# Optimization experiments

Measured on AMD Instinct MI355X. Metric: run time of the kernel, lower is better.

Reference implementation:

```python
import jax, jax.numpy as jnp
import numpy as np
import math

EPS = 1e-3  # numerical_stabilizer in relu_kernel_transformation


def setup_inputs() -> dict:
    key = jax.random.key(0)
    ks = jax.random.split(key, 6)
    B, L, DIM = 8, 4096, 768
    H, D, M = 12, 64, 256
    x = jax.random.normal(ks[0], (B, L, DIM), dtype=jnp.float32)
    qkv_w = jax.random.normal(ks[1], (3 * DIM, DIM), dtype=jnp.float32) * (DIM ** -0.5)
    qkv_b = jnp.zeros((3 * DIM,), dtype=jnp.float32)
    proj_w = jax.random.normal(ks[2], (DIM, DIM), dtype=jnp.float32) * (DIM ** -0.5)
    proj_b = jnp.zeros((DIM,), dtype=jnp.float32)
    # Gaussian orthogonal random matrix [M, D] (blocks of orthogonal rows, chi-scaled)
    blocks = []
    for i in range(M // D):
        g = jax.random.normal(ks[3 + 0] if False else jax.random.fold_in(ks[3], i), (D, D), dtype=jnp.float32)
        q, _ = jnp.linalg.qr(g)
        blocks.append(q.T)
    pm = jnp.concatenate(blocks, axis=0)  # [M, D]
    mult = jnp.linalg.norm(jax.random.normal(ks[4], (M, D), dtype=jnp.float32), axis=1)
    proj_mat = mult[:, None] * pm
    return {"x": x, "qkv_w": qkv_w, "qkv_b": qkv_b,
            "proj_w": proj_w, "proj_b": proj_b, "proj_mat": proj_mat}


def _relu_features(t, proj_mat):
    # t: [B, L, H, D], proj_mat: [M, D] -> [B, L, H, M]
    ratio = 1.0 / math.sqrt(float(proj_mat.shape[0]))
    z = ratio * jnp.einsum('blhd,md->blhm', t, proj_mat)
    return jax.nn.relu(z) + EPS


def reference(x, qkv_w, qkv_b, proj_w, proj_b, proj_mat):
    B, L, DIM = x.shape
    H = 12
    D = DIM // H
    qkv = x @ qkv_w.T + qkv_b                      # [B, L, 3*DIM]
    qkv = qkv.reshape(B, L, 3, H, D)
    q, k, v = qkv[:, :, 0], qkv[:, :, 1], qkv[:, :, 2]   # [B, L, H, D]
    q_p = _relu_features(q, proj_mat)              # [B, L, H, M]
    k_p = _relu_features(k, proj_mat)              # [B, L, H, M]
    # Non-causal FAVOR+ linear attention
    kv = jnp.einsum('blhm,blhd->bhmd', k_p, v)     # [B, H, M, D]
    k_sum = k_p.sum(axis=1)                        # [B, H, M]
    num = jnp.einsum('blhm,bhmd->blhd', q_p, kv)   # [B, L, H, D]
    den = jnp.einsum('blhm,bhm->blh', q_p, k_sum)  # [B, L, H]
    out = num / den[..., None]
    out = out.reshape(B, L, DIM)
    return out @ proj_w.T + proj_b
```

## Files before the change

kernel.cpp:

```cpp
#include <hip/hip_runtime.h>
#include <hip/hip_bf16.h>
#include <cstdint>

typedef __hip_bfloat16 bf16;
typedef short bf16x8 __attribute__((ext_vector_type(8)));
typedef float f32x4 __attribute__((ext_vector_type(4)));

#define RATIO 0.0625f
#define EPS_F 0.001f

__device__ __forceinline__ void unpack8(uint4 u, float* f) {
  f[0] = __uint_as_float(u.x << 16); f[1] = __uint_as_float(u.x & 0xffff0000u);
  f[2] = __uint_as_float(u.y << 16); f[3] = __uint_as_float(u.y & 0xffff0000u);
  f[4] = __uint_as_float(u.z << 16); f[5] = __uint_as_float(u.z & 0xffff0000u);
  f[6] = __uint_as_float(u.w << 16); f[7] = __uint_as_float(u.w & 0xffff0000u);
}

__device__ __forceinline__ unsigned short f2bf(float f) {
  unsigned int u = __float_as_uint(f);
  unsigned int r = (u + 0x7fffu + ((u >> 16) & 1u)) >> 16;
  return (unsigned short)r;
}

__device__ __forceinline__ void gload_lds16(const void* g, void* l) {
  __builtin_amdgcn_global_load_lds(
      (const __attribute__((address_space(1))) void*)(uintptr_t)g,
      (__attribute__((address_space(3))) void*)(uintptr_t)l, 16, 0, 0);
}

__global__ void zero_kernel(float* __restrict__ p, int n) {
  int i = blockIdx.x * 256 + threadIdx.x;
  if (i < n) p[i] = 0.f;
}

__global__ void conv_kernel(const float* __restrict__ src,
                            unsigned short* __restrict__ dst, long n) {
  long i = ((long)blockIdx.x * 256 + threadIdx.x) * 4;
  if (i < n) {
    float4 v = *(const float4*)(src + i);
    ushort4 o;
    o.x = f2bf(v.x); o.y = f2bf(v.y); o.z = f2bf(v.z); o.w = f2bf(v.w);
    *(ushort4*)(dst + i) = o;
  }
}

__device__ __forceinline__ void ds_read_B8(const short* Bb, int rB0, int l16,
                                           int quad, bf16x8 bfr[4][2]) {
  const int sw = l16 & 7;
#pragma unroll
  for (int ni = 0; ni < 4; ++ni)
#pragma unroll
    for (int ks = 0; ks < 2; ++ks)
      bfr[ni][ks] = *(const bf16x8*)
          &Bb[(rB0 + ni * 16 + l16) * 64 + (((ks * 4 + quad) ^ sw) * 8)];
}

template <int Q>
__device__ __forceinline__ void ds_read_A4(const short* Ab, int l16, int quad,
                                           bf16x8 af[2][2]) {
  const int sw = l16 & 7;
#pragma unroll
  for (int i = 0; i < 2; ++i)
#pragma unroll
    for (int ks = 0; ks < 2; ++ks)
      af[i][ks] = *(const bf16x8*)
          &Ab[((Q * 2 + i) * 16 + l16) * 64 + (((ks * 4 + quad) ^ sw) * 8)];
}

template <int Q>
__device__ __forceinline__ void mfma16(f32x4 acc[8][4], bf16x8 af[2][2],
                                       bf16x8 bfr[4][2]) {
#pragma unroll
  for (int i = 0; i < 2; ++i)
#pragma unroll
    for (int ni = 0; ni < 4; ++ni)
#pragma unroll
      for (int ks = 0; ks < 2; ++ks)
        acc[Q * 2 + i][ni] = __builtin_amdgcn_mfma_f32_16x16x32_bf16(
            af[i][ks], bfr[ni][ks], acc[Q * 2 + i][ni], 0, 0, 0);
}

template <bool OUT_F32>
__global__ __launch_bounds__(512, 2) void gemm_bt_kernel(
    const bf16* __restrict__ A, const bf16* __restrict__ Bt,
    const float* __restrict__ bias, void* __restrict__ Cout,
    int Ndim, int Kdim)
{
  __shared__ short lds[65536];
  const int tid = threadIdx.x;
  const int lane = tid & 63;
  const int w = tid >> 6;
  const int wr = w >> 2;
  const int wc = w & 3;
  const int quad = lane >> 4, l16 = lane & 15;

  int gx = gridDim.x;
  int nwg = gx * gridDim.y;
  int flat = blockIdx.y * gx + blockIdx.x;
  int qq = nwg >> 3, rr = nwg & 7;
  int xcd = flat & 7, sub = flat >> 3;
  int wg = (xcd < rr ? xcd * (qq + 1) : rr * (qq + 1) + (xcd - rr) * qq) + sub;
  long m0 = (long)(wg / gx) * 256;
  long n0 = (long)(wg % gx) * 256;

  const int r8 = lane >> 3;
  const int csw = ((lane & 7) ^ (r8 & 7)) * 8;
  const bf16* gAs = A + (m0 + (w >> 2) * 128 + (w & 3) * 8 + r8) * (long)Kdim + csw;
  const bf16* gBs = Bt + (n0 + w * 8 + r8) * (long)Kdim + csw;
  short* dA = &lds[(w >> 2) * 8192 + (w & 3) * 512];
  short* dB = &lds[32768 + w * 512];
  const long kb64 = 64L * Kdim;
  const long ka32 = 32L * Kdim;

  f32x4 acc[8][4];
#pragma unroll
  for (int i = 0; i < 8; i++)
#pragma unroll
    for (int j = 0; j < 4; j++)
      acc[i][j] = (f32x4){0.f, 0.f, 0.f, 0.f};

  const int NIT = Kdim >> 6;

#pragma unroll
  for (int j = 0; j < 4; ++j) gload_lds16(gBs + j * kb64, dB + j * 4096);
#pragma unroll
  for (int qa = 0; qa < 4; ++qa) gload_lds16(gAs + qa * ka32, dA + qa * 2048);
  asm volatile("s_waitcnt vmcnt(3)" ::: "memory");
  __builtin_amdgcn_s_barrier();

  bf16x8 bfr[4][2], af[2][2];

  for (int it = 0; it < NIT; ++it) {
    const int d = it & 1, nd = d ^ 1;
    const bool pf = (it < NIT - 1);
    const long kq1 = (long)(it + 1) * 64;
    const short* Ab = &lds[d * 16384 + wr * 8192];
    const short* Bb = &lds[32768 + d * 16384 + (wc >> 1) * 8192];
    const int rB0 = (wc & 1) * 64;
    short* dAn = dA + nd * 16384;
    short* dBn = dB + nd * 16384;

    ds_read_B8(Bb, rB0, l16, quad, bfr);
    ds_read_A4<0>(Ab, l16, quad, af);
    if (pf) {
      gload_lds16(gBs + kq1, dBn);
      gload_lds16(gBs + kb64 + kq1, dBn + 4096);
      asm volatile("s_waitcnt vmcnt(4)" ::: "memory");
    } else {
      asm volatile("s_waitcnt vmcnt(2)" ::: "memory");
    }
    asm volatile("s_waitcnt lgkmcnt(8)" ::: "memory");
    __builtin_amdgcn_s_barrier();
    asm volatile("s_waitcnt lgkmcnt(0)" ::: "memory");
    __builtin_amdgcn_sched_barrier(0);
    __builtin_amdgcn_s_setprio(1);
    mfma16<0>(acc, af, bfr);
    __builtin_amdgcn_s_setprio(0);
    __builtin_amdgcn_s_barrier();

    ds_read_A4<1>(Ab, l16, quad, af);
    if (pf) {
      gload_lds16(gBs + 2 * kb64 + kq1, dBn + 8192);
      gload_lds16(gBs + 3 * kb64 + kq1, dBn + 12288);
      asm volatile("s_waitcnt vmcnt(5)" ::: "memory");
    } else {
      asm volatile("s_waitcnt vmcnt(1)" ::: "memory");
    }
    __builtin_amdgcn_s_barrier();
    asm volatile("s_waitcnt lgkmcnt(0)" ::: "memory");
    __builtin_amdgcn_sched_barrier(0);
    __builtin_amdgcn_s_setprio(1);
    mfma16<1>(acc, af, bfr);
    __builtin_amdgcn_s_setprio(0);
    __builtin_amdgcn_s_barrier();

    ds_read_A4<2>(Ab, l16, quad, af);
    if (pf) {
      gload_lds16(gAs + kq1, dAn);
      gload_lds16(gAs + ka32 + kq1, dAn + 2048);
      asm volatile("s_waitcnt vmcnt(6)" ::: "memory");
    } else {
      asm volatile("s_waitcnt vmcnt(0)" ::: "memory");
    }
    __builtin_amdgcn_s_barrier();
    asm volatile("s_waitcnt lgkmcnt(0)" ::: "memory");
    __builtin_amdgcn_sched_barrier(0);
    __builtin_amdgcn_s_setprio(1);
    mfma16<2>(acc, af, bfr);
    __builtin_amdgcn_s_setprio(0);
    __builtin_amdgcn_s_barrier();

    ds_read_A4<3>(Ab, l16, quad, af);
    if (pf) {
      gload_lds16(gAs + 2 * ka32 + kq1, dAn + 4096);
      gload_lds16(gAs + 3 * ka32 + kq1, dAn + 6144);
      asm volatile("s_waitcnt vmcnt(3)" ::: "memory");
    }
    __builtin_amdgcn_s_barrier();
    asm volatile("s_waitcnt lgkmcnt(0)" ::: "memory");
    __builtin_amdgcn_sched_barrier(0);
    __builtin_amdgcn_s_setprio(1);
    mfma16<3>(acc, af, bfr);
    __builtin_amdgcn_s_setprio(0);
    __builtin_amdgcn_s_barrier();
  }

#pragma unroll
  for (int ni = 0; ni < 4; ++ni) {
    long col = n0 + wc * 64 + ni * 16 + l16;
    float bv = bias[col];
#pragma unroll
    for (int mi = 0; mi < 8; ++mi) {
      long row = m0 + wr * 128 + mi * 16 + quad * 4;
#pragma unroll
      for (int r = 0; r < 4; ++r) {
        float val = acc[mi][ni][r] + bv;
        if (OUT_F32)
          ((float*)Cout)[(row + r) * Ndim + col] = val;
        else
          ((bf16*)Cout)[(row + r) * Ndim + col] = __float2bfloat16(val);
      }
    }
  }
}

__global__ __launch_bounds__(256) void kv_mfma_kernel(
    const bf16* __restrict__ qkv, const bf16* __restrict__ pmb,
    float* __restrict__ kvbuf, float* __restrict__ ksumb)
{
  int bh = blockIdx.x;
  int b = bh / 12, h = bh % 12;
  int l0 = blockIdx.y * 1024;
  int tid = threadIdx.x, lane = tid & 63, w = tid >> 6;
  int quad = lane >> 4, l16 = lane & 15;

  __shared__ short k_lds[64 * 72];
  __shared__ short v_lds[64 * 72];
  __shared__ short kp3[256 * 72];

  f32x4 kvacc[4][4];
#pragma unroll
  for (int mt = 0; mt < 4; mt++)
#pragma unroll
    for (int dt = 0; dt < 4; dt++)
      kvacc[mt][dt] = (f32x4){0.f, 0.f, 0.f, 0.f};
  float ksum_r = 0.f;

  int srow = tid >> 2, sseg = (tid & 3) * 8;
  int swz = ((srow >> 3) & 3) << 4;

  for (int tile = 0; tile < 16; tile++) {
    long gr = ((long)(b * 4096 + l0 + tile * 64 + srow)) * 2304 + h * 64;
    uint4 kk0 = *(const uint4*)(qkv + gr + 768 + sseg);
    uint4 kk1 = *(const uint4*)(qkv + gr + 768 + sseg + 32);
    uint4 vv0 = *(const uint4*)(qkv + gr + 1536 + sseg);
    uint4 vv1 = *(const uint4*)(qkv + gr + 1536 + sseg + 32);
    __syncthreads();
    *(uint4*)&k_lds[srow * 72 + sseg] = kk0;
    *(uint4*)&k_lds[srow * 72 + sseg + 32] = kk1;
    *(uint4*)&v_lds[srow * 72 + (sseg ^ swz)] = vv0;
    *(uint4*)&v_lds[srow * 72 + ((sseg + 32) ^ swz)] = vv1;
    __syncthreads();

    bf16x8 af[4][2], bpm[4][2];
#pragma unroll
    for (int lt = 0; lt < 4; lt++)
#pragma unroll
      for (int ks = 0; ks < 2; ks++)
        af[lt][ks] = *(const bf16x8*)&k_lds[(lt * 16 + l16) * 72 + ks * 32 + quad * 8];
#pragma unroll
    for (int mt = 0; mt < 4; mt++)
#pragma unroll
      for (int ks = 0; ks < 2; ks++)
        bpm[mt][ks] = *(const bf16x8*)(pmb + (w * 64 + mt * 16 + l16) * 64 + ks * 32 + quad * 8);

#pragma unroll
    for (int lt = 0; lt < 4; lt++)
#pragma unroll
      for (int mt = 0; mt < 4; mt++) {
        f32x4 s = (f32x4){0.f, 0.f, 0.f, 0.f};
        s = __builtin_amdgcn_mfma_f32_16x16x32_bf16(af[lt][0], bpm[mt][0], s, 0, 0, 0);
        s = __builtin_amdgcn_mfma_f32_16x16x32_bf16(af[lt][1], bpm[mt][1], s, 0, 0, 0);
        ushort4 pk;
        pk.x = f2bf(fmaxf(s[0] * RATIO, 0.f) + EPS_F);
        pk.y = f2bf(fmaxf(s[1] * RATIO, 0.f) + EPS_F);
        pk.z = f2bf(fmaxf(s[2] * RATIO, 0.f) + EPS_F);
        pk.w = f2bf(fmaxf(s[3] * RATIO, 0.f) + EPS_F);
        *(ushort4*)&kp3[(w * 64 + mt * 16 + l16) * 72 + lt * 16 + quad * 4] = pk;
      }
    __syncthreads();

#pragma unroll
    for (int j8 = 0; j8 < 8; j8++) {
      uint4 u = *(const uint4*)&kp3[tid * 72 + j8 * 8];
      float f[8]; unpack8(u, f);
      ksum_r += ((f[0] + f[1]) + (f[2] + f[3])) + ((f[4] + f[5]) + (f[6] + f[7]));
    }

#pragma unroll
    for (int ls = 0; ls < 2; ls++) {
      bf16x8 a2[4];
#pragma unroll
      for (int mt = 0; mt < 4; mt++)
        a2[mt] = *(const bf16x8*)&kp3[(w * 64 + mt * 16 + l16) * 72 + ls * 32 + quad * 8];
#pragma unroll
      for (int dt = 0; dt < 4; dt++) {
        bf16x8 b2;
        int dcol = (dt * 16 + l16) ^ (quad << 4);
#pragma unroll
        for (int jj = 0; jj < 8; jj++)
          b2[jj] = v_lds[(ls * 32 + quad * 8 + jj) * 72 + dcol];
#pragma unroll
        for (int mt = 0; mt < 4; mt++)
          kvacc[mt][dt] = __builtin_amdgcn_mfma_f32_16x16x32_bf16(a2[mt], b2, kvacc[mt][dt], 0, 0, 0);
      }
    }
  }

#pragma unroll
  for (int mt = 0; mt < 4; mt++)
#pragma unroll
    for (int dt = 0; dt < 4; dt++)
#pragma unroll
      for (int r = 0; r < 4; r++)
        atomicAdd(kvbuf + ((long)bh * 64 + dt * 16 + l16) * 256 + w * 64 + mt * 16 + quad * 4 + r,
                  kvacc[mt][dt][r]);
  atomicAdd(ksumb + bh * 256 + tid, ksum_r);
}

__global__ __launch_bounds__(256) void attn_mfma_kernel(
    const bf16* __restrict__ qkv, const bf16* __restrict__ pmb,
    const bf16* __restrict__ kvtb, const float* __restrict__ ksumb,
    bf16* __restrict__ attn)
{
  int bh = blockIdx.x;
  int b = bh / 12, h = bh % 12;
  int l0 = blockIdx.y * 64;
  int tid = threadIdx.x, lane = tid & 63, w = tid >> 6;
  int quad = lane >> 4, l16 = lane & 15;

  __shared__ short q_lds[64 * 72];
  __shared__ short qp2[64 * 264];
  __shared__ short kvt_lds[64 * 264];
  __shared__ float ksum_lds[256];
  __shared__ float den_part[4][64];

  {
    int srow = tid >> 2, sseg = (tid & 3) * 8;
    long gr = ((long)(b * 4096 + l0 + srow)) * 2304 + h * 64;
    *(uint4*)&q_lds[srow * 72 + sseg]      = *(const uint4*)(qkv + gr + sseg);
    *(uint4*)&q_lds[srow * 72 + sseg + 32] = *(const uint4*)(qkv + gr + sseg + 32);
  }
  {
    int row = tid >> 2, cb = (tid & 3) * 64;
    const bf16* src = kvtb + (long)bh * 16384 + row * 256 + cb;
    short* dst = &kvt_lds[row * 264 + cb];
#pragma unroll
    for (int j = 0; j < 8; j++)
      *(uint4*)(dst + j * 8) = *(const uint4*)(src + j * 8);
  }
  ksum_lds[tid] = ksumb[bh * 256 + tid];
  __syncthreads();

  {
    bf16x8 apm[4][2], bq[4][2];
#pragma unroll
    for (int mt = 0; mt < 4; mt++)
#pragma unroll
      for (int ks = 0; ks < 2; ks++)
        apm[mt][ks] = *(const bf16x8*)(pmb + (w * 64 + mt * 16 + l16) * 64 + ks * 32 + quad * 8);
#pragma unroll
    for (int lt = 0; lt < 4; lt++)
#pragma unroll
      for (int ks = 0; ks < 2; ks++)
        bq[lt][ks] = *(const bf16x8*)&q_lds[(lt * 16 + l16) * 72 + ks * 32 + quad * 8];

#pragma unroll
    for (int mt = 0; mt < 4; mt++)
#pragma unroll
      for (int lt = 0; lt < 4; lt++) {
        f32x4 s = (f32x4){0.f, 0.f, 0.f, 0.f};
        s = __builtin_amdgcn_mfma_f32_16x16x32_bf16(apm[mt][0], bq[lt][0], s, 0, 0, 0);
        s = __builtin_amdgcn_mfma_f32_16x16x32_bf16(apm[mt][1], bq[lt][1], s, 0, 0, 0);
        ushort4 pk;
        pk.x = f2bf(fmaxf(s[0] * RATIO, 0.f) + EPS_F);
        pk.y = f2bf(fmaxf(s[1] * RATIO, 0.f) + EPS_F);
        pk.z = f2bf(fmaxf(s[2] * RATIO, 0.f) + EPS_F);
        pk.w = f2bf(fmaxf(s[3] * RATIO, 0.f) + EPS_F);
        *(ushort4*)&qp2[(lt * 16 + l16) * 264 + w * 64 + mt * 16 + quad * 4] = pk;
      }
  }
  __syncthreads();

  {
    int l = tid & 63, Q = tid >> 6;
    float dp = 0.f;
#pragma unroll
    for (int j8 = 0; j8 < 8; j8++) {
      uint4 u = *(const uint4*)&qp2[l * 264 + Q * 64 + j8 * 8];
      float f[8]; unpack8(u, f);
#pragma unroll
      for (int i = 0; i < 8; i++) dp += f[i] * ksum_lds[Q * 64 + j8 * 8 + i];
    }
    den_part[Q][l] = dp;
  }

  f32x4 o[4];
#pragma unroll
  for (int dt = 0; dt < 4; dt++) o[dt] = (f32x4){0.f, 0.f, 0.f, 0.f};
#pragma unroll
  for (int ms = 0; ms < 8; ms++) {
    bf16x8 aq = *(const bf16x8*)&qp2[(w * 16 + l16) * 264 + ms * 32 + quad * 8];
#pragma unroll
    for (int dt = 0; dt < 4; dt++) {
      bf16x8 bk = *(const bf16x8*)&kvt_lds[(dt * 16 + l16) * 264 + ms * 32 + quad * 8];
      o[dt] = __builtin_amdgcn_mfma_f32_16x16x32_bf16(aq, bk, o[dt], 0, 0, 0);
    }
  }
  __syncthreads();

  float rden[4];
#pragma unroll
  for (int r = 0; r < 4; r++) {
    int l = w * 16 + quad * 4 + r;
    rden[r] = 1.f / (den_part[0][l] + den_part[1][l] + den_part[2][l] + den_part[3][l]);
  }
#pragma unroll
  for (int dt = 0; dt < 4; dt++)
#pragma unroll
    for (int r = 0; r < 4; r++) {
      int l = w * 16 + quad * 4 + r;
      attn[((long)(b * 4096 + l0 + l)) * 768 + h * 64 + dt * 16 + l16] =
          __float2bfloat16(o[dt][r] * rden[r]);
    }
}

extern "C" void kernel_launch(void* const* d_in, const int* in_sizes, int n_in,
                              void* d_out, int out_size, void* d_ws, size_t ws_size,
                              hipStream_t stream)
{
  const float* x      = (const float*)d_in[0];
  const float* qkv_w  = (const float*)d_in[1];
  const float* qkv_b  = (const float*)d_in[2];
  const float* proj_w = (const float*)d_in[3];
  const float* proj_b = (const float*)d_in[4];
  const float* pmat   = (const float*)d_in[5];
  float* out = (float*)d_out;

  char* ws = (char*)d_ws;
  bf16*  qkv   = (bf16*)ws;
  bf16*  xbuf  = (bf16*)(ws + 150994944);
  bf16*  attn  = xbuf;
  float* kvbuf = (float*)(ws + 201326592);
  float* ksumb = (float*)(ws + 207618048);
  bf16*  wqkv  = (bf16*)(ws + 207716352);
  bf16*  kvtb  = (bf16*)(ws + 207716352);
  bf16*  pmb   = (bf16*)(ws + 210862080);
  bf16*  wproj = (bf16*)(ws + 211255296);

  int nz = 96 * 64 * 256 + 96 * 256;
  zero_kernel<<<dim3((nz + 255) / 256), 256, 0, stream>>>(kvbuf, nz);

  conv_kernel<<<dim3(25165824 / 1024), 256, 0, stream>>>(x, (unsigned short*)xbuf, 25165824L);
  conv_kernel<<<dim3(1769472 / 1024), 256, 0, stream>>>(qkv_w, (unsigned short*)wqkv, 1769472L);
  conv_kernel<<<dim3(589824 / 1024), 256, 0, stream>>>(proj_w, (unsigned short*)wproj, 589824L);

  gemm_bt_kernel<false><<<dim3(2304 / 256, 32768 / 256), 512, 0, stream>>>(
      xbuf, wqkv, qkv_b, qkv, 2304, 768);

  conv_kernel<<<dim3(16384 / 1024), 256, 0, stream>>>(pmat, (unsigned short*)pmb, 16384L);

  kv_mfma_kernel<<<dim3(96, 4), 256, 0, stream>>>(qkv, pmb, kvbuf, ksumb);

  conv_kernel<<<dim3(1572864 / 1024), 256, 0, stream>>>(kvbuf, (unsigned short*)kvtb, 1572864L);

  attn_mfma_kernel<<<dim3(96, 64), 256, 0, stream>>>(qkv, pmb, kvtb, ksumb, attn);

  gemm_bt_kernel<true><<<dim3(768 / 256, 32768 / 256), 512, 0, stream>>>(
      attn, wproj, proj_b, out, 768, 768);
}
```

Measured before the change: 609.5 us.

## Split KV reduction over feature blocks instead of sequence chunks, drop atomics

```diff
diff --git a/kernel.cpp b/kernel.cpp
--- a/kernel.cpp
+++ b/kernel.cpp
@@ -26,11 +26,6 @@
   __builtin_amdgcn_global_load_lds(
       (const __attribute__((address_space(1))) void*)(uintptr_t)g,
       (__attribute__((address_space(3))) void*)(uintptr_t)l, 16, 0, 0);
-}
-
-__global__ void zero_kernel(float* __restrict__ p, int n) {
-  int i = blockIdx.x * 256 + threadIdx.x;
-  if (i < n) p[i] = 0.f;
 }
 
 __global__ void conv_kernel(const float* __restrict__ src,
@@ -230,27 +225,33 @@
 {
   int bh = blockIdx.x;
   int b = bh / 12, h = bh % 12;
-  int l0 = blockIdx.y * 1024;
+  int mb = blockIdx.y * 64;
   int tid = threadIdx.x, lane = tid & 63, w = tid >> 6;
   int quad = lane >> 4, l16 = lane & 15;
 
   __shared__ short k_lds[64 * 72];
   __shared__ short v_lds[64 * 72];
-  __shared__ short kp3[256 * 72];
-
-  f32x4 kvacc[4][4];
+  __shared__ short kp3[64 * 72];
+  __shared__ float red[4][64];
+
+  bf16x8 bpm[4][2];
 #pragma unroll
   for (int mt = 0; mt < 4; mt++)
 #pragma unroll
-    for (int dt = 0; dt < 4; dt++)
-      kvacc[mt][dt] = (f32x4){0.f, 0.f, 0.f, 0.f};
+    for (int ks = 0; ks < 2; ks++)
+      bpm[mt][ks] = *(const bf16x8*)(pmb + (mb + mt * 16 + l16) * 64 + ks * 32 + quad * 8);
+
+  f32x4 kvacc[4];
+#pragma unroll
+  for (int mt = 0; mt < 4; mt++) kvacc[mt] = (f32x4){0.f, 0.f, 0.f, 0.f};
   float ksum_r = 0.f;
 
   int srow = tid >> 2, sseg = (tid & 3) * 8;
   int swz = ((srow >> 3) & 3) << 4;
-
-  for (int tile = 0; tile < 16; tile++) {
-    long gr = ((long)(b * 4096 + l0 + tile * 64 + srow)) * 2304 + h * 64;
+  int mm = tid & 63, lq = tid >> 6;
+
+  for (int tile = 0; tile < 64; tile++) {
+    long gr = ((long)(b * 4096 + tile * 64 + srow)) * 2304 + h * 64;
     uint4 kk0 = *(const uint4*)(qkv + gr + 768 + sseg);
     uint4 kk1 = *(const uint4*)(qkv + gr + 768 + sseg + 32);
     uint4 vv0 = *(const uint4*)(qkv + gr + 1536 + sseg);
@@ -262,37 +263,29 @@
     *(uint4*)&v_lds[srow * 72 + ((sseg + 32) ^ swz)] = vv1;
     __syncthreads();
 
-    bf16x8 af[4][2], bpm[4][2];
-#pragma unroll
-    for (int lt = 0; lt < 4; lt++)
+    {
+      bf16x8 af[2];
 #pragma unroll
       for (int ks = 0; ks < 2; ks++)
-        af[lt][ks] = *(const bf16x8*)&k_lds[(lt * 16 + l16) * 72 + ks * 32 + quad * 8];
-#pragma unroll
-    for (int mt = 0; mt < 4; mt++)
-#pragma unroll
-      for (int ks = 0; ks < 2; ks++)
-        bpm[mt][ks] = *(const bf16x8*)(pmb + (w * 64 + mt * 16 + l16) * 64 + ks * 32 + quad * 8);
-
-#pragma unroll
-    for (int lt = 0; lt < 4; lt++)
+        af[ks] = *(const bf16x8*)&k_lds[(w * 16 + l16) * 72 + ks * 32 + quad * 8];
 #pragma unroll
       for (int mt = 0; mt < 4; mt++) {
         f32x4 s = (f32x4){0.f, 0.f, 0.f, 0.f};
-        s = __builtin_amdgcn_mfma_f32_16x16x32_bf16(af[lt][0], bpm[mt][0], s, 0, 0, 0);
-        s = __builtin_amdgcn_mfma_f32_16x16x32_bf16(af[lt][1], bpm[mt][1], s, 0, 0, 0);
+        s = __builtin_amdgcn_mfma_f32_16x16x32_bf16(af[0], bpm[mt][0], s, 0, 0, 0);
+        s = __builtin_amdgcn_mfma_f32_16x16x32_bf16(af[1], bpm[mt][1], s, 0, 0, 0);
         ushort4 pk;
         pk.x = f2bf(fmaxf(s[0] * RATIO, 0.f) + EPS_F);
         pk.y = f2bf(fmaxf(s[1] * RATIO, 0.f) + EPS_F);
         pk.z = f2bf(fmaxf(s[2] * RATIO, 0.f) + EPS_F);
         pk.w = f2bf(fmaxf(s[3] * RATIO, 0.f) + EPS_F);
-        *(ushort4*)&kp3[(w * 64 + mt * 16 + l16) * 72 + lt * 16 + quad * 4] = pk;
+        *(ushort4*)&kp3[(mt * 16 + l16) * 72 + w * 16 + quad * 4] = pk;
       }
+    }
     __syncthreads();
 
 #pragma unroll
-    for (int j8 = 0; j8 < 8; j8++) {
-      uint4 u = *(const uint4*)&kp3[tid * 72 + j8 * 8];
+    for (int j = 0; j < 2; j++) {
+      uint4 u = *(const uint4*)&kp3[mm * 72 + lq * 16 + j * 8];
       float f[8]; unpack8(u, f);
       ksum_r += ((f[0] + f[1]) + (f[2] + f[3])) + ((f[4] + f[5]) + (f[6] + f[7]));
     }
@@ -302,30 +295,30 @@
       bf16x8 a2[4];
 #pragma unroll
       for (int mt = 0; mt < 4; mt++)
-        a2[mt] = *(const bf16x8*)&kp3[(w * 64 + mt * 16 + l16) * 72 + ls * 32 + quad * 8];
-#pragma unroll
-      for (int dt = 0; dt < 4; dt++) {
-        bf16x8 b2;
-        int dcol = (dt * 16 + l16) ^ (quad << 4);
-#pragma unroll
-        for (int jj = 0; jj < 8; jj++)
-          b2[jj] = v_lds[(ls * 32 + quad * 8 + jj) * 72 + dcol];
-#pragma unroll
-        for (int mt = 0; mt < 4; mt++)
-          kvacc[mt][dt] = __builtin_amdgcn_mfma_f32_16x16x32_bf16(a2[mt], b2, kvacc[mt][dt], 0, 0, 0);
-      }
+        a2[mt] = *(const bf16x8*)&kp3[(mt * 16 + l16) * 72 + ls * 32 + quad * 8];
+      bf16x8 b2;
+      int dcol = (w * 16 + l16) ^ (quad << 4);
+#pragma unroll
+      for (int jj = 0; jj < 8; jj++)
+        b2[jj] = v_lds[(ls * 32 + quad * 8 + jj) * 72 + dcol];
+#pragma unroll
+      for (int mt = 0; mt < 4; mt++)
+        kvacc[mt] = __builtin_amdgcn_mfma_f32_16x16x32_bf16(a2[mt], b2, kvacc[mt], 0, 0, 0);
     }
   }
 
 #pragma unroll
   for (int mt = 0; mt < 4; mt++)
 #pragma unroll
-    for (int dt = 0; dt < 4; dt++)
-#pragma unroll
-      for (int r = 0; r < 4; r++)
-        atomicAdd(kvbuf + ((long)bh * 64 + dt * 16 + l16) * 256 + w * 64 + mt * 16 + quad * 4 + r,
-                  kvacc[mt][dt][r]);
-  atomicAdd(ksumb + bh * 256 + tid, ksum_r);
+    for (int r = 0; r < 4; r++)
+      kvbuf[(long)bh * 16384 + (w * 16 + l16) * 256 + mb + mt * 16 + quad * 4 + r] =
+          kvacc[mt][r];
+
+  red[lq][mm] = ksum_r;
+  __syncthreads();
+  if (tid < 64)
+    ksumb[bh * 256 + mb + tid] =
+        (red[0][tid] + red[1][tid]) + (red[2][tid] + red[3][tid]);
 }
 
 __global__ __launch_bounds__(256) void attn_mfma_kernel(
@@ -458,9 +451,6 @@
   bf16*  pmb   = (bf16*)(ws + 210862080);
   bf16*  wproj = (bf16*)(ws + 211255296);
 
-  int nz = 96 * 64 * 256 + 96 * 256;
-  zero_kernel<<<dim3((nz + 255) / 256), 256, 0, stream>>>(kvbuf, nz);
-
   conv_kernel<<<dim3(25165824 / 1024), 256, 0, stream>>>(x, (unsigned short*)xbuf, 25165824L);
   conv_kernel<<<dim3(1769472 / 1024), 256, 0, stream>>>(qkv_w, (unsigned short*)wqkv, 1769472L);
   conv_kernel<<<dim3(589824 / 1024), 256, 0, stream>>>(proj_w, (unsigned short*)wproj, 589824L);
```

Result: faster. 561.0 us (-8.0%).
